# Performance work log

Hardware: AMD Instinct MI355X
Metric: run time of the kernel (lower is better)

## Reference

```python
import jax, jax.numpy as jnp
import numpy as np

B, T, C, H = 512, 40, 512, 512


def _gru_dir(x, Wih, Whh, bih, bhh):
    """Single-direction PyTorch-convention GRU. x: [B,T,C] -> [B,T,H]."""
    Hh = Whh.shape[1]
    # precompute input projections for all timesteps: [B,T,3H]
    gx = jnp.einsum('btc,gc->btg', x, Wih) + bih

    def step(h, gxt):
        gh = h @ Whh.T + bhh  # [B,3H]
        r = jax.nn.sigmoid(gxt[:, :Hh] + gh[:, :Hh])
        z = jax.nn.sigmoid(gxt[:, Hh:2 * Hh] + gh[:, Hh:2 * Hh])
        n = jnp.tanh(gxt[:, 2 * Hh:] + r * gh[:, 2 * Hh:])
        h_new = (1.0 - z) * n + z * h
        return h_new, h_new

    h0 = jnp.zeros((x.shape[0], Hh), x.dtype)
    _, ys = jax.lax.scan(step, h0, jnp.swapaxes(gx, 0, 1))  # [T,B,H]
    return jnp.swapaxes(ys, 0, 1)


def setup_inputs() -> dict:
    key = jax.random.key(0)
    ks = jax.random.split(key, 10)
    s = 1.0 / np.sqrt(H)  # PyTorch default init scale
    lengths = jax.random.randint(ks[0], (B,), 5, T + 1)
    valid = jnp.arange(T)[None, :] < lengths[:, None]  # [B,T]
    ref_expr = jax.random.normal(ks[1], (B, T, C), jnp.float32) * valid[..., None]
    mk = lambda k, shape: jax.random.uniform(k, shape, jnp.float32, -s, s)
    return {
        'ref_expr': ref_expr,
        'Wih_f': mk(ks[2], (3 * H, C)), 'Whh_f': mk(ks[3], (3 * H, H)),
        'bih_f': mk(ks[4], (3 * H,)), 'bhh_f': mk(ks[5], (3 * H,)),
        'Wih_b': mk(ks[6], (3 * H, C)), 'Whh_b': mk(ks[7], (3 * H, H)),
        'bih_b': mk(ks[8], (3 * H,)), 'bhh_b': mk(ks[9], (3 * H,)),
    }


def reference(ref_expr, Wih_f, Whh_f, bih_f, bhh_f, Wih_b, Whh_b, bih_b, bhh_b):
    # padded positions are all-zero embedding vectors -> masked out
    valid = jnp.any(ref_expr != 0, axis=-1)  # [B,T], True = keep
    y_fwd = _gru_dir(ref_expr, Wih_f, Whh_f, bih_f, bhh_f)
    y_bwd = _gru_dir(ref_expr[:, ::-1], Wih_b, Whh_b, bih_b, bhh_b)[:, ::-1]
    y_word = jnp.concatenate([y_fwd, y_bwd], axis=-1)  # [B,T,2H]
    # masked max pooling over valid tokens (output_type='max')
    neg = jnp.finfo(y_word.dtype).min
    y = jnp.max(jnp.where(valid[..., None], y_word, neg), axis=1, keepdims=True)
    return y  # [B,1,2H]
```

## Files before the change

### kernel.cpp

```cpp
#include <hip/hip_runtime.h>
#include <hip/hip_bf16.h>
#include <float.h>

#define BB 512
#define TT 40
#define CC 512
#define HH 512

typedef short bf16x8 __attribute__((ext_vector_type(8)));
typedef float f32x4 __attribute__((ext_vector_type(4)));
typedef unsigned short ushortx8 __attribute__((ext_vector_type(8)));

#define LDSH 49152
#define LDSF 98304
#define LDSTOT 98320

__device__ __forceinline__ unsigned short f2bf(float f){
  union { float f; unsigned int i; } v; v.f = f;
  unsigned int r = v.i + 0x7fffu + ((v.i >> 16) & 1u);
  return (unsigned short)(r >> 16);
}

__device__ __forceinline__ bf16x8 load_sc0(const unsigned short* p){
  bf16x8 r;
  asm volatile("global_load_dwordx4 %0, %1, off sc0" : "=v"(r) : "v"(p));
  return r;
}
#define WAITV(N) do { asm volatile("s_waitcnt vmcnt(" #N ")" ::: "memory"); \
                      __builtin_amdgcn_sched_barrier(0); } while(0)

__device__ __forceinline__ void waitv_idx(int n){
  switch(n){
    case 0:  WAITV(0);  break;  case 1:  WAITV(1);  break;
    case 2:  WAITV(2);  break;  case 3:  WAITV(3);  break;
    case 4:  WAITV(4);  break;  case 5:  WAITV(5);  break;
    case 6:  WAITV(6);  break;  case 7:  WAITV(7);  break;
    case 8:  WAITV(8);  break;  case 9:  WAITV(9);  break;
    case 10: WAITV(10); break;  case 11: WAITV(11); break;
    case 12: WAITV(12); break;  case 13: WAITV(13); break;
    case 14: WAITV(14); break;  default: WAITV(15); break;
  }
}

__device__ __forceinline__ float fast_sigmoid(float x){
  return __builtin_amdgcn_rcpf(1.f + __expf(-x));
}
__device__ __forceinline__ float fast_tanh(float x){
  return 1.f - 2.f*__builtin_amdgcn_rcpf(__expf(2.f*x) + 1.f);
}

__global__ void prep_x_kernel(const float* __restrict__ x, unsigned short* __restrict__ xb,
                              float* __restrict__ maskT){
  int w = blockIdx.x*4 + (threadIdx.x>>6);
  int lane = threadIdx.x & 63;
  const float* src = x + (size_t)w*CC + lane*8;
  f32x4 a = *(const f32x4*)(src);
  f32x4 b = *(const f32x4*)(src+4);
  ushortx8 o;
  o[0]=f2bf(a[0]); o[1]=f2bf(a[1]); o[2]=f2bf(a[2]); o[3]=f2bf(a[3]);
  o[4]=f2bf(b[0]); o[5]=f2bf(b[1]); o[6]=f2bf(b[2]); o[7]=f2bf(b[3]);
  *(ushortx8*)(xb + (size_t)w*CC + lane*8) = o;
  bool nz = (a[0]!=0.f)||(a[1]!=0.f)||(a[2]!=0.f)||(a[3]!=0.f)||
            (b[0]!=0.f)||(b[1]!=0.f)||(b[2]!=0.f)||(b[3]!=0.f);
  unsigned long long bal = __ballot(nz);
  if (lane==0){
    int b_ = w / TT, t_ = w % TT;
    maskT[t_*BB + b_] = bal ? 1.0f : 0.0f;
  }
}

__global__ void cvt_kernel(const float* __restrict__ src, unsigned short* __restrict__ dst, int n8){
  int i = blockIdx.x*blockDim.x + threadIdx.x;
  if (i < n8){
    f32x4 a = *(const f32x4*)(src + i*8);
    f32x4 b = *(const f32x4*)(src + i*8 + 4);
    ushortx8 o;
    o[0]=f2bf(a[0]); o[1]=f2bf(a[1]); o[2]=f2bf(a[2]); o[3]=f2bf(a[3]);
    o[4]=f2bf(b[0]); o[5]=f2bf(b[1]); o[6]=f2bf(b[2]); o[7]=f2bf(b[3]);
    *(ushortx8*)(dst + i*8) = o;
  }
}

__global__ void init_h_kernel(unsigned short* __restrict__ hb, unsigned int* __restrict__ flags){
  int i = blockIdx.x*blockDim.x + threadIdx.x;
  hb[i] = 0;
  if (i < 256) flags[i] = 0u;
}

__global__ __launch_bounds__(512, 2) void gru_persist_kernel(
    const unsigned short* __restrict__ xb,
    const unsigned short* __restrict__ wihF, const unsigned short* __restrict__ whhF,
    const unsigned short* __restrict__ wihB, const unsigned short* __restrict__ whhB,
    const float* __restrict__ bihF, const float* __restrict__ bhhF,
    const float* __restrict__ bihB, const float* __restrict__ bhhB,
    const float* __restrict__ maskT,
    unsigned short* __restrict__ hb,
    float* __restrict__ out, unsigned int* __restrict__ flags)
{
  const int bid   = blockIdx.x;
  const int grp   = bid & 7;
  const int strip = bid >> 3;
  const int dir   = grp >> 2;
  const int bslab = grp & 3;
  const int b0 = bslab * 128;
  const int n0 = strip * 16;
  unsigned int* fl = flags + grp*32;

  const unsigned short* wih = dir ? wihB : wihF;
  const unsigned short* whh = dir ? whhB : whhF;
  const float* bih = dir ? bihB : bihF;
  const float* bhh = dir ? bhhB : bhhF;

  const int tid  = threadIdx.x;
  const int lane = tid & 63;
  const int lr   = lane & 15;
  const int lkg  = lane >> 4;
  const int wv   = tid >> 6;
  const int wrow = wv * 16;

  __shared__ __align__(16) char smem[LDSTOT];
  unsigned int* arrive = (unsigned int*)(smem + LDSF);

  for (int q = tid; q < 6144; q += 512) {
    const int p_  = q >= 3072;
    const int r_  = p_ ? (q - 3072) : q;
    const int row = r_ >> 6;
    const int kc  = (r_ & 63) * 8;
    const unsigned short* src =
        (p_ ? whh : wih) + ((size_t)((row>>4)*HH + n0 + (row&15)))*512 + kc;
    *(ushortx8*)(smem + p_*LDSH + row*1024 + ((kc*2) ^ ((row&15)<<4))) =
        *(const ushortx8*)src;
  }
  if (tid == 0) arrive[0] = 0u;
  __syncthreads();

  const int jj = n0 + lr;
  const float br  = bih[jj]        + bhh[jj];
  const float bz  = bih[HH + jj]   + bhh[HH + jj];
  const float bnx = bih[2*HH + jj];
  const float bnh = bhh[2*HH + jj];

  float omax[4], hreg[4];
  #pragma unroll
  for (int j=0; j<4; ++j){ omax[j] = -FLT_MAX; hreg[j] = 0.f; }

  const int swz = lr << 4;
  const char* wbx = smem + lr*1024;
  const char* wbh = smem + LDSH + lr*1024;

  for (int t = 0; t < TT; ++t) {
    const int tx = dir ? (TT-1-t) : t;
    const int bi = t & 1;
    const unsigned short* hbin = hb + (size_t)(dir*2 + bi)      * (BB*HH);
    unsigned short* hbout      = hb + (size_t)(dir*2 + (bi^1))  * (BB*HH);

    f32x4 ar = 0.f, az = 0.f, anx = 0.f, anh = 0.f;

    const unsigned short* xr0 = xb + ((size_t)(b0 + wrow + lr)*TT + tx)*CC;

    #pragma unroll
    for (int kk = 0; kk < 16; ++kk) {
      const int ko = kk*32 + lkg*8;
      bf16x8 a0 = *(const bf16x8*)(xr0 + ko);
      const int kbx = (ko*2) ^ swz;
      bf16x8 brf = *(const bf16x8*)(wbx +         kbx);
      bf16x8 bzf = *(const bf16x8*)(wbx + 16384 + kbx);
      bf16x8 bnf = *(const bf16x8*)(wbx + 32768 + kbx);
      ar  = __builtin_amdgcn_mfma_f32_16x16x32_bf16(a0, brf, ar,0,0,0);
      az  = __builtin_amdgcn_mfma_f32_16x16x32_bf16(a0, bzf, az,0,0,0);
      anx = __builtin_amdgcn_mfma_f32_16x16x32_bf16(a0, bnf, anx,0,0,0);
    }

    const f32x4 mk = *(const f32x4*)(maskT + tx*BB + b0 + wrow + lkg*4);

    if (t > 0) {
      const unsigned int tgt = (unsigned)t;
      unsigned int spin = 0;
      for (;;) {
        unsigned int v = tgt;
        if (lane < 32)
          v = __hip_atomic_load(&fl[lane], __ATOMIC_RELAXED, __HIP_MEMORY_SCOPE_AGENT);
        if (__ballot(v < tgt) == 0ull) break;
        if (++spin >= (1u<<22)) break;
        __builtin_amdgcn_s_sleep(1);
      }
    }

    WAITV(0);

    const unsigned short* hr0 = hbin + (size_t)(b0 + wrow + lr)*HH;
    bf16x8 ph[16];
    #pragma unroll
    for (int q = 0; q < 16; ++q)
      ph[q] = load_sc0(hr0 + q*32 + lkg*8);
    #pragma unroll
    for (int kk = 0; kk < 16; ++kk) {
      const int ko = kk*32 + lkg*8;
      const int kbx = (ko*2) ^ swz;
      bf16x8 brf = *(const bf16x8*)(wbh +         kbx);
      bf16x8 bzf = *(const bf16x8*)(wbh + 16384 + kbx);
      bf16x8 bnf = *(const bf16x8*)(wbh + 32768 + kbx);
      waitv_idx(15 - kk);
      bf16x8 c0 = ph[kk];
      ar  = __builtin_amdgcn_mfma_f32_16x16x32_bf16(c0, brf, ar,0,0,0);
      az  = __builtin_amdgcn_mfma_f32_16x16x32_bf16(c0, bzf, az,0,0,0);
      anh = __builtin_amdgcn_mfma_f32_16x16x32_bf16(c0, bnf, anh,0,0,0);
    }

    #pragma unroll
    for (int j=0; j<4; ++j){
      const int b = b0 + wrow + lkg*4 + j;
      const float rg = fast_sigmoid(ar[j] + br);
      const float zg = fast_sigmoid(az[j] + bz);
      const float ng = fast_tanh(anx[j] + bnx + rg*(anh[j] + bnh));
      const float hn = (1.f - zg)*ng + zg*hreg[j];
      hreg[j] = hn;
      hbout[(size_t)b*HH + jj] = f2bf(hn);
      const float cand = (mk[j] != 0.f) ? hn : -FLT_MAX;
      omax[j] = fmaxf(omax[j], cand);
    }

    if (t < TT-1) {
      WAITV(0);
      if (lane == 0) {
        unsigned int prev =
            __hip_atomic_fetch_add(arrive, 1u, __ATOMIC_ACQ_REL, __HIP_MEMORY_SCOPE_WORKGROUP);
        if (prev + 1u == 8u*(unsigned)(t+1))
          __hip_atomic_store(&fl[strip], (unsigned)(t+1),
                             __ATOMIC_RELAXED, __HIP_MEMORY_SCOPE_AGENT);
      }
    }
  }

  #pragma unroll
  for (int j=0; j<4; ++j){
    const int b = b0 + wrow + lkg*4 + j;
    out[(size_t)b*(2*HH) + dir*HH + jj] = omax[j];
  }
}

extern "C" void kernel_launch(void* const* d_in, const int* in_sizes, int n_in,
                              void* d_out, int out_size, void* d_ws, size_t ws_size,
                              hipStream_t stream) {
  const float* x    = (const float*)d_in[0];
  const float* WihF = (const float*)d_in[1];
  const float* WhhF = (const float*)d_in[2];
  const float* bihF = (const float*)d_in[3];
  const float* bhhF = (const float*)d_in[4];
  const float* WihB = (const float*)d_in[5];
  const float* WhhB = (const float*)d_in[6];
  const float* bihB = (const float*)d_in[7];
  const float* bhhB = (const float*)d_in[8];
  float* out = (float*)d_out;

  char* ws = (char*)d_ws;
  unsigned short* xb    = (unsigned short*)(ws);
  unsigned short* wb    = (unsigned short*)(ws + 20971520);
  unsigned short* wihFb = wb;
  unsigned short* whhFb = wb + 786432;
  unsigned short* wihBb = wb + 2*786432;
  unsigned short* whhBb = wb + 3*786432;
  float* maskT = (float*)(ws + 27262976);
  unsigned short* hb = (unsigned short*)(ws + 27344896);
  unsigned int* flags = (unsigned int*)(ws + 29442048);

  prep_x_kernel<<<BB*TT/4, 256, 0, stream>>>(x, xb, maskT);
  cvt_kernel<<<384, 256, 0, stream>>>(WihF, wihFb, 98304);
  cvt_kernel<<<384, 256, 0, stream>>>(WhhF, whhFb, 98304);
  cvt_kernel<<<384, 256, 0, stream>>>(WihB, wihBb, 98304);
  cvt_kernel<<<384, 256, 0, stream>>>(WhhB, whhBb, 98304);
  init_h_kernel<<<4096, 256, 0, stream>>>(hb, flags);

  gru_persist_kernel<<<256, 512, 0, stream>>>(xb, wihFb, whhFb, wihBb, whhBb,
                                              bihF, bhhF, bihB, bhhB,
                                              maskT, hb, out, flags);
}
```

Before: 339.2 us.

## Precompute input projections before recurrence and pair both directions per block

Adds a fused persistent kernel. Each block first computes the input-gate projections for all 40 timesteps with Wih held in LDS and writes them to a bf16 workspace buffer. It then reloads LDS with Whh and runs the recurrence, reading the precomputed projections so the serial step only does the hidden-state matmul. Each block now covers both directions over 64 batch rows, and the four waves of each direction signal completion through an LDS counter before publishing a global flag. This takes the input GEMM off the latency-critical step chain, at the cost of about 120MB of extra workspace traffic and bf16 rounding of the projections. The new path runs only when the workspace is large enough.

```diff
diff --git a/kernel.cpp b/kernel.cpp
--- a/kernel.cpp
+++ b/kernel.cpp
@@ -84,7 +84,204 @@
 __global__ void init_h_kernel(unsigned short* __restrict__ hb, unsigned int* __restrict__ flags){
   int i = blockIdx.x*blockDim.x + threadIdx.x;
   hb[i] = 0;
-  if (i < 256) flags[i] = 0u;
+  if (i < 512) flags[i] = 0u;
+}
+
+__global__ __launch_bounds__(512, 2) void gru_fused_kernel(
+    const unsigned short* __restrict__ xb,
+    const unsigned short* __restrict__ wihF, const unsigned short* __restrict__ whhF,
+    const unsigned short* __restrict__ wihB, const unsigned short* __restrict__ whhB,
+    const float* __restrict__ bihF, const float* __restrict__ bhhF,
+    const float* __restrict__ bihB, const float* __restrict__ bhhB,
+    const float* __restrict__ maskT,
+    unsigned short* __restrict__ hb,
+    float* __restrict__ out, unsigned int* __restrict__ flags,
+    unsigned short* __restrict__ gx)
+{
+  const int bid   = blockIdx.x;
+  const int grp   = bid & 7;
+  const int strip = bid >> 3;
+  const int b0 = grp * 64;
+  const int n0 = strip * 16;
+
+  const int tid  = threadIdx.x;
+  const int lane = tid & 63;
+  const int lr   = lane & 15;
+  const int lkg  = lane >> 4;
+  const int wv   = tid >> 6;
+  const int dir  = wv >> 2;
+  const int wq   = wv & 3;
+
+  const float* bih = dir ? bihB : bihF;
+  const float* bhh = dir ? bhhB : bhhF;
+
+  __shared__ __align__(16) char smem[LDSTOT];
+  unsigned int* arr = (unsigned int*)(smem + LDSF);
+
+  const int swz = lr << 4;
+
+  for (int q = tid; q < 6144; q += 512) {
+    const int p_  = q >= 3072;
+    const int r_  = p_ ? (q - 3072) : q;
+    const int row = r_ >> 6;
+    const int kc  = (r_ & 63) * 8;
+    const unsigned short* src =
+        (p_ ? wihB : wihF) + ((size_t)((row>>4)*HH + n0 + (row&15)))*512 + kc;
+    *(ushortx8*)(smem + p_*LDSH + row*1024 + ((kc*2) ^ ((row&15)<<4))) =
+        *(const ushortx8*)src;
+  }
+  __syncthreads();
+
+  const char* wpan = smem + dir*LDSH + lr*1024;
+  unsigned short* gxw = gx + (size_t)bid*245760 + (size_t)dir*122880;
+
+  for (int tb = 0; tb < 10; ++tb) {
+    f32x4 acc[4][3];
+    #pragma unroll
+    for (int u=0; u<4; ++u){ acc[u][0]=0.f; acc[u][1]=0.f; acc[u][2]=0.f; }
+    const unsigned short* xr = xb + ((size_t)(b0 + wq*16 + lr)*TT + tb*4)*CC;
+    #pragma unroll
+    for (int kk = 0; kk < 16; ++kk) {
+      const int ko = kk*32 + lkg*8;
+      const int kbx = (ko*2) ^ swz;
+      bf16x8 brf = *(const bf16x8*)(wpan +         kbx);
+      bf16x8 bzf = *(const bf16x8*)(wpan + 16384 + kbx);
+      bf16x8 bnf = *(const bf16x8*)(wpan + 32768 + kbx);
+      #pragma unroll
+      for (int u=0; u<4; ++u){
+        bf16x8 a0 = *(const bf16x8*)(xr + u*CC + ko);
+        acc[u][0] = __builtin_amdgcn_mfma_f32_16x16x32_bf16(a0, brf, acc[u][0],0,0,0);
+        acc[u][1] = __builtin_amdgcn_mfma_f32_16x16x32_bf16(a0, bzf, acc[u][1],0,0,0);
+        acc[u][2] = __builtin_amdgcn_mfma_f32_16x16x32_bf16(a0, bnf, acc[u][2],0,0,0);
+      }
+    }
+    #pragma unroll
+    for (int u=0; u<4; ++u){
+      #pragma unroll
+      for (int g=0; g<3; ++g){
+        uint2 pk;
+        pk.x = (unsigned)f2bf(acc[u][g][0]) | ((unsigned)f2bf(acc[u][g][1]) << 16);
+        pk.y = (unsigned)f2bf(acc[u][g][2]) | ((unsigned)f2bf(acc[u][g][3]) << 16);
+        const size_t idx = ((size_t)((tb*4+u)*3 + g)*16 + lr)*64 + wq*16 + lkg*4;
+        *(uint2*)((char*)gxw + idx*2) = pk;
+      }
+    }
+  }
+  __syncthreads();
+
+  for (int q = tid; q < 6144; q += 512) {
+    const int p_  = q >= 3072;
+    const int r_  = p_ ? (q - 3072) : q;
+    const int row = r_ >> 6;
+    const int kc  = (r_ & 63) * 8;
+    const unsigned short* src =
+        (p_ ? whhB : whhF) + ((size_t)((row>>4)*HH + n0 + (row&15)))*512 + kc;
+    *(ushortx8*)(smem + p_*LDSH + row*1024 + ((kc*2) ^ ((row&15)<<4))) =
+        *(const ushortx8*)src;
+  }
+  if (tid < 2) arr[tid] = 0u;
+  __syncthreads();
+
+  const int jj = n0 + lr;
+  const float br  = bih[jj]        + bhh[jj];
+  const float bz  = bih[HH + jj]   + bhh[HH + jj];
+  const float bnx = bih[2*HH + jj];
+  const float bnh = bhh[2*HH + jj];
+
+  unsigned int* fl = flags + (dir*8 + grp)*32;
+  unsigned int* myarr = arr + dir;
+
+  float omax[4], hreg[4];
+  #pragma unroll
+  for (int j=0; j<4; ++j){ omax[j] = -FLT_MAX; hreg[j] = 0.f; }
+
+  for (int t = 0; t < TT; ++t) {
+    const int tx = dir ? (TT-1-t) : t;
+    const int bi = t & 1;
+    const unsigned short* hbin = hb + (size_t)(dir*2 + bi)      * (BB*HH);
+    unsigned short* hbout      = hb + (size_t)(dir*2 + (bi^1))  * (BB*HH);
+
+    const f32x4 mk = *(const f32x4*)(maskT + tx*BB + b0 + wq*16 + lkg*4);
+    uint2 ug[3];
+    #pragma unroll
+    for (int g=0; g<3; ++g){
+      const size_t idx = ((size_t)(tx*3 + g)*16 + lr)*64 + wq*16 + lkg*4;
+      ug[g] = *(const uint2*)((const char*)gxw + idx*2);
+    }
+
+    if (t > 0) {
+      const unsigned int tgt = (unsigned)t;
+      unsigned int spin = 0;
+      for (;;) {
+        unsigned int v = tgt;
+        if (lane < 32)
+          v = __hip_atomic_load(&fl[lane], __ATOMIC_RELAXED, __HIP_MEMORY_SCOPE_AGENT);
+        if (__ballot(v < tgt) == 0ull) break;
+        if (++spin >= (1u<<24)) break;
+        __builtin_amdgcn_s_sleep(1);
+      }
+    }
+    WAITV(0);
+
+    const unsigned short* hr0 = hbin + (size_t)(b0 + wq*16 + lr)*HH;
+    bf16x8 ph[16];
+    #pragma unroll
+    for (int q = 0; q < 16; ++q)
+      ph[q] = load_sc0(hr0 + q*32 + lkg*8);
+
+    f32x4 ar = 0.f, az = 0.f, anh = 0.f;
+    #pragma unroll
+    for (int kk = 0; kk < 16; ++kk) {
+      const int ko = kk*32 + lkg*8;
+      const int kbx = (ko*2) ^ swz;
+      bf16x8 brf = *(const bf16x8*)(wpan +         kbx);
+      bf16x8 bzf = *(const bf16x8*)(wpan + 16384 + kbx);
+      bf16x8 bnf = *(const bf16x8*)(wpan + 32768 + kbx);
+      waitv_idx(15 - kk);
+      bf16x8 c0 = ph[kk];
+      ar  = __builtin_amdgcn_mfma_f32_16x16x32_bf16(c0, brf, ar,0,0,0);
+      az  = __builtin_amdgcn_mfma_f32_16x16x32_bf16(c0, bzf, az,0,0,0);
+      anh = __builtin_amdgcn_mfma_f32_16x16x32_bf16(c0, bnf, anh,0,0,0);
+    }
+
+    float gxf[3][4];
+    #pragma unroll
+    for (int g=0; g<3; ++g){
+      gxf[g][0] = __uint_as_float(ug[g].x << 16);
+      gxf[g][1] = __uint_as_float(ug[g].x & 0xffff0000u);
+      gxf[g][2] = __uint_as_float(ug[g].y << 16);
+      gxf[g][3] = __uint_as_float(ug[g].y & 0xffff0000u);
+    }
+    #pragma unroll
+    for (int j=0; j<4; ++j){
+      const int b = b0 + wq*16 + lkg*4 + j;
+      const float rg = fast_sigmoid(ar[j] + gxf[0][j] + br);
+      const float zg = fast_sigmoid(az[j] + gxf[1][j] + bz);
+      const float ng = fast_tanh(gxf[2][j] + bnx + rg*(anh[j] + bnh));
+      const float hn = (1.f - zg)*ng + zg*hreg[j];
+      hreg[j] = hn;
+      hbout[(size_t)b*HH + jj] = f2bf(hn);
+      const float cand = (mk[j] != 0.f) ? hn : -FLT_MAX;
+      omax[j] = fmaxf(omax[j], cand);
+    }
+
+    if (t < TT-1) {
+      WAITV(0);
+      if (lane == 0) {
+        unsigned int prev =
+            __hip_atomic_fetch_add(myarr, 1u, __ATOMIC_ACQ_REL, __HIP_MEMORY_SCOPE_WORKGROUP);
+        if (prev + 1u == 4u*(unsigned)(t+1))
+          __hip_atomic_store(&fl[strip], (unsigned)(t+1),
+                             __ATOMIC_RELAXED, __HIP_MEMORY_SCOPE_AGENT);
+      }
+    }
+  }
+
+  #pragma unroll
+  for (int j=0; j<4; ++j){
+    const int b = b0 + wq*16 + lkg*4 + j;
+    out[(size_t)b*(2*HH) + dir*HH + jj] = omax[j];
+  }
 }
 
 __global__ __launch_bounds__(512, 2) void gru_persist_kernel(
@@ -155,7 +352,6 @@
     unsigned short* hbout      = hb + (size_t)(dir*2 + (bi^1))  * (BB*HH);
 
     f32x4 ar = 0.f, az = 0.f, anx = 0.f, anh = 0.f;
-
     const unsigned short* xr0 = xb + ((size_t)(b0 + wrow + lr)*TT + tx)*CC;
 
     #pragma unroll
@@ -185,7 +381,6 @@
         __builtin_amdgcn_s_sleep(1);
       }
     }
-
     WAITV(0);
 
     const unsigned short* hr0 = hbin + (size_t)(b0 + wrow + lr)*HH;
@@ -263,6 +458,7 @@
   float* maskT = (float*)(ws + 27262976);
   unsigned short* hb = (unsigned short*)(ws + 27344896);
   unsigned int* flags = (unsigned int*)(ws + 29442048);
+  unsigned short* gx  = (unsigned short*)(ws + 29444096);
 
   prep_x_kernel<<<BB*TT/4, 256, 0, stream>>>(x, xb, maskT);
   cvt_kernel<<<384, 256, 0, stream>>>(WihF, wihFb, 98304);
@@ -271,7 +467,14 @@
   cvt_kernel<<<384, 256, 0, stream>>>(WhhB, whhBb, 98304);
   init_h_kernel<<<4096, 256, 0, stream>>>(hb, flags);
 
-  gru_persist_kernel<<<256, 512, 0, stream>>>(xb, wihFb, whhFb, wihBb, whhBb,
+  const size_t need = 29444096ull + 125829120ull;
+  if (ws_size >= need) {
+    gru_fused_kernel<<<256, 512, 0, stream>>>(xb, wihFb, whhFb, wihBb, whhBb,
                                               bihF, bhhF, bihB, bhhB,
-                                              maskT, hb, out, flags);
-}
+                                              maskT, hb, out, flags, gx);
+  } else {
+    gru_persist_kernel<<<256, 512, 0, stream>>>(xb, wihFb, whhFb, wihBb, whhBb,
+                                                bihF, bhhF, bihB, bhhB,
+                                                maskT, hb, out, flags);
+  }
+}
```

Result: slower. 702.1 us (+107.0%).

## Batch input projections for four timesteps into LDS ahead of recurrence

Applied to the files above, without the earlier changes.

Restructures the time loop into windows of four steps. Each window first computes the x·Wih projections for all four timesteps at once, reusing each LDS weight fragment across four MFMAs, and stores the results to a new LDS region as bf16. The sequential recurrent steps then read these precomputed values, so the critical path between cross-block flag waits holds only the h·Whh GEMM and the gate math. The costs are roughly 48KB more LDS per block, extra bf16 rounding of the input projections, a longer spin timeout, and a wider flag-clear loop.

```diff
diff --git a/kernel.cpp b/kernel.cpp
--- a/kernel.cpp
+++ b/kernel.cpp
@@ -12,8 +12,9 @@
 typedef unsigned short ushortx8 __attribute__((ext_vector_type(8)));
 
 #define LDSH 49152
-#define LDSF 98304
-#define LDSTOT 98320
+#define LDSG 98304
+#define LDSF 147456
+#define LDSTOT 147472
 
 __device__ __forceinline__ unsigned short f2bf(float f){
   union { float f; unsigned int i; } v; v.f = f;
@@ -84,7 +85,7 @@
 __global__ void init_h_kernel(unsigned short* __restrict__ hb, unsigned int* __restrict__ flags){
   int i = blockIdx.x*blockDim.x + threadIdx.x;
   hb[i] = 0;
-  if (i < 256) flags[i] = 0u;
+  if (i < 512) flags[i] = 0u;
 }
 
 __global__ __launch_bounds__(512, 2) void gru_persist_kernel(
@@ -148,86 +149,119 @@
   const char* wbx = smem + lr*1024;
   const char* wbh = smem + LDSH + lr*1024;
 
-  for (int t = 0; t < TT; ++t) {
-    const int tx = dir ? (TT-1-t) : t;
-    const int bi = t & 1;
-    const unsigned short* hbin = hb + (size_t)(dir*2 + bi)      * (BB*HH);
-    unsigned short* hbout      = hb + (size_t)(dir*2 + (bi^1))  * (BB*HH);
-
-    f32x4 ar = 0.f, az = 0.f, anx = 0.f, anh = 0.f;
-
-    const unsigned short* xr0 = xb + ((size_t)(b0 + wrow + lr)*TT + tx)*CC;
+  for (int w = 0; w < 10; ++w) {
+    {
+      f32x4 gacc[4][3];
+      #pragma unroll
+      for (int u=0; u<4; ++u){ gacc[u][0]=0.f; gacc[u][1]=0.f; gacc[u][2]=0.f; }
+      const unsigned short* xr[4];
+      #pragma unroll
+      for (int u=0; u<4; ++u){
+        const int txu = dir ? (TT-1-(w*4+u)) : (w*4+u);
+        xr[u] = xb + ((size_t)(b0 + wrow + lr)*TT + txu)*CC;
+      }
+      #pragma unroll
+      for (int kk = 0; kk < 16; ++kk) {
+        const int ko = kk*32 + lkg*8;
+        const int kbx = (ko*2) ^ swz;
+        bf16x8 brf = *(const bf16x8*)(wbx +         kbx);
+        bf16x8 bzf = *(const bf16x8*)(wbx + 16384 + kbx);
+        bf16x8 bnf = *(const bf16x8*)(wbx + 32768 + kbx);
+        #pragma unroll
+        for (int u=0; u<4; ++u){
+          bf16x8 a0 = *(const bf16x8*)(xr[u] + ko);
+          gacc[u][0] = __builtin_amdgcn_mfma_f32_16x16x32_bf16(a0, brf, gacc[u][0],0,0,0);
+          gacc[u][1] = __builtin_amdgcn_mfma_f32_16x16x32_bf16(a0, bzf, gacc[u][1],0,0,0);
+          gacc[u][2] = __builtin_amdgcn_mfma_f32_16x16x32_bf16(a0, bnf, gacc[u][2],0,0,0);
+        }
+      }
+      #pragma unroll
+      for (int u=0; u<4; ++u)
+        #pragma unroll
+        for (int g=0; g<3; ++g){
+          uint2 pk;
+          pk.x = (unsigned)f2bf(gacc[u][g][0]) | ((unsigned)f2bf(gacc[u][g][1]) << 16);
+          pk.y = (unsigned)f2bf(gacc[u][g][2]) | ((unsigned)f2bf(gacc[u][g][3]) << 16);
+          *(uint2*)(smem + LDSG + (((u*3+g)<<9) + tid)*8) = pk;
+        }
+    }
 
     #pragma unroll
-    for (int kk = 0; kk < 16; ++kk) {
-      const int ko = kk*32 + lkg*8;
-      bf16x8 a0 = *(const bf16x8*)(xr0 + ko);
-      const int kbx = (ko*2) ^ swz;
-      bf16x8 brf = *(const bf16x8*)(wbx +         kbx);
-      bf16x8 bzf = *(const bf16x8*)(wbx + 16384 + kbx);
-      bf16x8 bnf = *(const bf16x8*)(wbx + 32768 + kbx);
-      ar  = __builtin_amdgcn_mfma_f32_16x16x32_bf16(a0, brf, ar,0,0,0);
-      az  = __builtin_amdgcn_mfma_f32_16x16x32_bf16(a0, bzf, az,0,0,0);
-      anx = __builtin_amdgcn_mfma_f32_16x16x32_bf16(a0, bnf, anx,0,0,0);
-    }
-
-    const f32x4 mk = *(const f32x4*)(maskT + tx*BB + b0 + wrow + lkg*4);
-
-    if (t > 0) {
-      const unsigned int tgt = (unsigned)t;
-      unsigned int spin = 0;
-      for (;;) {
-        unsigned int v = tgt;
-        if (lane < 32)
-          v = __hip_atomic_load(&fl[lane], __ATOMIC_RELAXED, __HIP_MEMORY_SCOPE_AGENT);
-        if (__ballot(v < tgt) == 0ull) break;
-        if (++spin >= (1u<<22)) break;
-        __builtin_amdgcn_s_sleep(1);
-      }
-    }
-
-    WAITV(0);
-
-    const unsigned short* hr0 = hbin + (size_t)(b0 + wrow + lr)*HH;
-    bf16x8 ph[16];
-    #pragma unroll
-    for (int q = 0; q < 16; ++q)
-      ph[q] = load_sc0(hr0 + q*32 + lkg*8);
-    #pragma unroll
-    for (int kk = 0; kk < 16; ++kk) {
-      const int ko = kk*32 + lkg*8;
-      const int kbx = (ko*2) ^ swz;
-      bf16x8 brf = *(const bf16x8*)(wbh +         kbx);
-      bf16x8 bzf = *(const bf16x8*)(wbh + 16384 + kbx);
-      bf16x8 bnf = *(const bf16x8*)(wbh + 32768 + kbx);
-      waitv_idx(15 - kk);
-      bf16x8 c0 = ph[kk];
-      ar  = __builtin_amdgcn_mfma_f32_16x16x32_bf16(c0, brf, ar,0,0,0);
-      az  = __builtin_amdgcn_mfma_f32_16x16x32_bf16(c0, bzf, az,0,0,0);
-      anh = __builtin_amdgcn_mfma_f32_16x16x32_bf16(c0, bnf, anh,0,0,0);
-    }
-
-    #pragma unroll
-    for (int j=0; j<4; ++j){
-      const int b = b0 + wrow + lkg*4 + j;
-      const float rg = fast_sigmoid(ar[j] + br);
-      const float zg = fast_sigmoid(az[j] + bz);
-      const float ng = fast_tanh(anx[j] + bnx + rg*(anh[j] + bnh));
-      const float hn = (1.f - zg)*ng + zg*hreg[j];
-      hreg[j] = hn;
-      hbout[(size_t)b*HH + jj] = f2bf(hn);
-      const float cand = (mk[j] != 0.f) ? hn : -FLT_MAX;
-      omax[j] = fmaxf(omax[j], cand);
-    }
-
-    if (t < TT-1) {
+    for (int u = 0; u < 4; ++u) {
+      const int t  = w*4 + u;
+      const int tx = dir ? (TT-1-t) : t;
+      const int bi = t & 1;
+      const unsigned short* hbin = hb + (size_t)(dir*2 + bi)      * (BB*HH);
+      unsigned short* hbout      = hb + (size_t)(dir*2 + (bi^1))  * (BB*HH);
+
+      const f32x4 mk = *(const f32x4*)(maskT + tx*BB + b0 + wrow + lkg*4);
+
+      if (t > 0) {
+        const unsigned int tgt = (unsigned)t;
+        unsigned int spin = 0;
+        for (;;) {
+          unsigned int v = tgt;
+          if (lane < 32)
+            v = __hip_atomic_load(&fl[lane], __ATOMIC_RELAXED, __HIP_MEMORY_SCOPE_AGENT);
+          if (__ballot(v < tgt) == 0ull) break;
+          if (++spin >= (1u<<24)) break;
+          __builtin_amdgcn_s_sleep(1);
+        }
+      }
       WAITV(0);
-      if (lane == 0) {
-        unsigned int prev =
-            __hip_atomic_fetch_add(arrive, 1u, __ATOMIC_ACQ_REL, __HIP_MEMORY_SCOPE_WORKGROUP);
-        if (prev + 1u == 8u*(unsigned)(t+1))
-          __hip_atomic_store(&fl[strip], (unsigned)(t+1),
-                             __ATOMIC_RELAXED, __HIP_MEMORY_SCOPE_AGENT);
+
+      const unsigned short* hr0 = hbin + (size_t)(b0 + wrow + lr)*HH;
+      bf16x8 ph[16];
+      #pragma unroll
+      for (int q = 0; q < 16; ++q)
+        ph[q] = load_sc0(hr0 + q*32 + lkg*8);
+
+      f32x4 ar = 0.f, az = 0.f, anh = 0.f;
+      #pragma unroll
+      for (int kk = 0; kk < 16; ++kk) {
+        const int ko = kk*32 + lkg*8;
+        const int kbx = (ko*2) ^ swz;
+        bf16x8 brf = *(const bf16x8*)(wbh +         kbx);
+        bf16x8 bzf = *(const bf16x8*)(wbh + 16384 + kbx);
+        bf16x8 bnf = *(const bf16x8*)(wbh + 32768 + kbx);
+        waitv_idx(15 - kk);
+        bf16x8 c0 = ph[kk];
+        ar  = __builtin_amdgcn_mfma_f32_16x16x32_bf16(c0, brf, ar,0,0,0);
+        az  = __builtin_amdgcn_mfma_f32_16x16x32_bf16(c0, bzf, az,0,0,0);
+        anh = __builtin_amdgcn_mfma_f32_16x16x32_bf16(c0, bnf, anh,0,0,0);
+      }
+
+      float gxf[3][4];
+      #pragma unroll
+      for (int g=0; g<3; ++g){
+        const uint2 ug = *(const uint2*)(smem + LDSG + (((u*3+g)<<9) + tid)*8);
+        gxf[g][0] = __uint_as_float(ug.x << 16);
+        gxf[g][1] = __uint_as_float(ug.x & 0xffff0000u);
+        gxf[g][2] = __uint_as_float(ug.y << 16);
+        gxf[g][3] = __uint_as_float(ug.y & 0xffff0000u);
+      }
+      #pragma unroll
+      for (int j=0; j<4; ++j){
+        const int b = b0 + wrow + lkg*4 + j;
+        const float rg = fast_sigmoid(ar[j] + gxf[0][j] + br);
+        const float zg = fast_sigmoid(az[j] + gxf[1][j] + bz);
+        const float ng = fast_tanh(gxf[2][j] + bnx + rg*(anh[j] + bnh));
+        const float hn = (1.f - zg)*ng + zg*hreg[j];
+        hreg[j] = hn;
+        hbout[(size_t)b*HH + jj] = f2bf(hn);
+        const float cand = (mk[j] != 0.f) ? hn : -FLT_MAX;
+        omax[j] = fmaxf(omax[j], cand);
+      }
+
+      if (t < TT-1) {
+        WAITV(0);
+        if (lane == 0) {
+          unsigned int prev =
+              __hip_atomic_fetch_add(arrive, 1u, __ATOMIC_ACQ_REL, __HIP_MEMORY_SCOPE_WORKGROUP);
+          if (prev + 1u == 8u*(unsigned)(t+1))
+            __hip_atomic_store(&fl[strip], (unsigned)(t+1),
+                               __ATOMIC_RELAXED, __HIP_MEMORY_SCOPE_AGENT);
+        }
       }
     }
   }
```

Result: slower. 510.0 us (+50.4%).

## Split each block across both directions with 64-row batch slabs and global Wih reads

Applied to the files above, without the earlier changes.

Each workgroup now handles both GRU directions: waves 0-3 run forward and waves 4-7 run backward over a 64-row batch slab, rather than one direction over 128 rows. LDS now holds both directions' recurrent Whh tiles, and the input-projection weights Wih are read straight from global memory (L2) instead of LDS. Sync groups double to 16 with per-direction arrival counters, and the spin cap is raised. This spreads per-block recurrent work over more independent groups, each waiting on fewer producers, at the cost of extra global traffic for the Wih reads in the non-recurrent part of each step.

```diff
diff --git a/kernel.cpp b/kernel.cpp
--- a/kernel.cpp
+++ b/kernel.cpp
@@ -84,7 +84,7 @@
 __global__ void init_h_kernel(unsigned short* __restrict__ hb, unsigned int* __restrict__ flags){
   int i = blockIdx.x*blockDim.x + threadIdx.x;
   hb[i] = 0;
-  if (i < 256) flags[i] = 0u;
+  if (i < 512) flags[i] = 0u;
 }
 
 __global__ __launch_bounds__(512, 2) void gru_persist_kernel(
@@ -98,28 +98,28 @@
     float* __restrict__ out, unsigned int* __restrict__ flags)
 {
   const int bid   = blockIdx.x;
-  const int grp   = bid & 7;
+  const int slab  = bid & 7;
   const int strip = bid >> 3;
-  const int dir   = grp >> 2;
-  const int bslab = grp & 3;
-  const int b0 = bslab * 128;
+  const int b0 = slab * 64;
   const int n0 = strip * 16;
-  unsigned int* fl = flags + grp*32;
-
-  const unsigned short* wih = dir ? wihB : wihF;
-  const unsigned short* whh = dir ? whhB : whhF;
-  const float* bih = dir ? bihB : bihF;
-  const float* bhh = dir ? bhhB : bhhF;
 
   const int tid  = threadIdx.x;
   const int lane = tid & 63;
   const int lr   = lane & 15;
   const int lkg  = lane >> 4;
   const int wv   = tid >> 6;
-  const int wrow = wv * 16;
+  const int dir  = wv >> 2;
+  const int wq   = wv & 3;
+  const int wrow = wq * 16;
+
+  const unsigned short* wih = dir ? wihB : wihF;
+  const float* bih = dir ? bihB : bihF;
+  const float* bhh = dir ? bhhB : bhhF;
+
+  unsigned int* fl = flags + (dir*8 + slab)*32;
 
   __shared__ __align__(16) char smem[LDSTOT];
-  unsigned int* arrive = (unsigned int*)(smem + LDSF);
+  unsigned int* arr = (unsigned int*)(smem + LDSF);
 
   for (int q = tid; q < 6144; q += 512) {
     const int p_  = q >= 3072;
@@ -127,11 +127,11 @@
     const int row = r_ >> 6;
     const int kc  = (r_ & 63) * 8;
     const unsigned short* src =
-        (p_ ? whh : wih) + ((size_t)((row>>4)*HH + n0 + (row&15)))*512 + kc;
+        (p_ ? whhB : whhF) + ((size_t)((row>>4)*HH + n0 + (row&15)))*512 + kc;
     *(ushortx8*)(smem + p_*LDSH + row*1024 + ((kc*2) ^ ((row&15)<<4))) =
         *(const ushortx8*)src;
   }
-  if (tid == 0) arrive[0] = 0u;
+  if (tid < 2) arr[tid] = 0u;
   __syncthreads();
 
   const int jj = n0 + lr;
@@ -145,8 +145,11 @@
   for (int j=0; j<4; ++j){ omax[j] = -FLT_MAX; hreg[j] = 0.f; }
 
   const int swz = lr << 4;
-  const char* wbx = smem + lr*1024;
-  const char* wbh = smem + LDSH + lr*1024;
+  const char* wbh = smem + dir*LDSH + lr*1024;
+  const unsigned short* wxr = wih + ((size_t)(0*HH + n0 + lr))*CC;
+  const unsigned short* wxz = wih + ((size_t)(1*HH + n0 + lr))*CC;
+  const unsigned short* wxn = wih + ((size_t)(2*HH + n0 + lr))*CC;
+  unsigned int* myarr = arr + dir;
 
   for (int t = 0; t < TT; ++t) {
     const int tx = dir ? (TT-1-t) : t;
@@ -161,11 +164,10 @@
     #pragma unroll
     for (int kk = 0; kk < 16; ++kk) {
       const int ko = kk*32 + lkg*8;
-      bf16x8 a0 = *(const bf16x8*)(xr0 + ko);
-      const int kbx = (ko*2) ^ swz;
-      bf16x8 brf = *(const bf16x8*)(wbx +         kbx);
-      bf16x8 bzf = *(const bf16x8*)(wbx + 16384 + kbx);
-      bf16x8 bnf = *(const bf16x8*)(wbx + 32768 + kbx);
+      bf16x8 a0  = *(const bf16x8*)(xr0 + ko);
+      bf16x8 brf = *(const bf16x8*)(wxr + ko);
+      bf16x8 bzf = *(const bf16x8*)(wxz + ko);
+      bf16x8 bnf = *(const bf16x8*)(wxn + ko);
       ar  = __builtin_amdgcn_mfma_f32_16x16x32_bf16(a0, brf, ar,0,0,0);
       az  = __builtin_amdgcn_mfma_f32_16x16x32_bf16(a0, bzf, az,0,0,0);
       anx = __builtin_amdgcn_mfma_f32_16x16x32_bf16(a0, bnf, anx,0,0,0);
@@ -181,11 +183,10 @@
         if (lane < 32)
           v = __hip_atomic_load(&fl[lane], __ATOMIC_RELAXED, __HIP_MEMORY_SCOPE_AGENT);
         if (__ballot(v < tgt) == 0ull) break;
-        if (++spin >= (1u<<22)) break;
+        if (++spin >= (1u<<24)) break;
         __builtin_amdgcn_s_sleep(1);
       }
     }
-
     WAITV(0);
 
     const unsigned short* hr0 = hbin + (size_t)(b0 + wrow + lr)*HH;
@@ -224,8 +225,8 @@
       WAITV(0);
       if (lane == 0) {
         unsigned int prev =
-            __hip_atomic_fetch_add(arrive, 1u, __ATOMIC_ACQ_REL, __HIP_MEMORY_SCOPE_WORKGROUP);
-        if (prev + 1u == 8u*(unsigned)(t+1))
+            __hip_atomic_fetch_add(myarr, 1u, __ATOMIC_ACQ_REL, __HIP_MEMORY_SCOPE_WORKGROUP);
+        if (prev + 1u == 4u*(unsigned)(t+1))
           __hip_atomic_store(&fl[strip], (unsigned)(t+1),
                              __ATOMIC_RELAXED, __HIP_MEMORY_SCOPE_AGENT);
       }
```

Measured after the change: 623.8 us. 1.84x slower.
